# Kernel tuning notes

Measured on AMD Instinct MI355X. Metric: run time of the kernel, lower is better.

Reference implementation:

```python
import jax, jax.numpy as jnp
import numpy as np

EPS = 1e-5  # torch BatchNorm1d default eps

def _bn(x, g, b):
    # BatchNorm1d in training mode: batch mean, biased variance
    m = jnp.mean(x, axis=0)
    v = jnp.mean((x - m) ** 2, axis=0)
    return g * (x - m) * jax.lax.rsqrt(v + EPS) + b

N_ENT, N_REL = 50000, 200
D_E = D_R = 32
RANK = 32
NI = 1024  # must satisfy NI**2 == D_R * D_E**3
B = 64

def setup_inputs() -> dict:
    key = jax.random.key(0)
    ks = jax.random.split(key, 10)
    s = 0.001
    inp = {
        "E": s * jax.random.normal(ks[0], (N_ENT, D_E), jnp.float32),
        "R": s * jax.random.normal(ks[1], (N_REL, D_R), jnp.float32),
        "U_root": s * jax.random.normal(ks[2], (N_REL, RANK, RANK), jnp.float32),
        "U12": s * jax.random.normal(ks[3], (RANK, NI, NI), jnp.float32),
        "U3R": s * jax.random.normal(ks[4], (RANK, NI, NI), jnp.float32),
        "P": s * jax.random.normal(ks[5], (RANK, D_E), jnp.float32),
        "g_r": jnp.ones((D_R,), jnp.float32), "b_r": jnp.zeros((D_R,), jnp.float32),
        "g_e": jnp.ones((D_E,), jnp.float32), "b_e": jnp.zeros((D_E,), jnp.float32),
        "g_w": jnp.ones((D_E,), jnp.float32), "b_w": jnp.zeros((D_E,), jnp.float32),
        "r_idx": jax.random.randint(ks[6], (B,), 0, N_REL),
        "e2_idx": jax.random.randint(ks[7], (B,), 0, N_ENT),
        "e3_idx": jax.random.randint(ks[8], (B,), 0, N_ENT),
        "miss_ent_domain": 3,
    }
    return inp

def reference(E, R, U_root, U12, U3R, P, g_r, b_r, g_e, b_e, g_w, b_w,
              r_idx, e2_idx, e3_idx, miss_ent_domain):
    Bsz = r_idx.shape[0]
    d_r, d_e = R.shape[1], E.shape[1]

    r_emb = _bn(R[r_idx], g_r, b_r)                      # (B, d_r)

    # einsum 'brs,ria,rjb,rkc->bijk' with P.unsqueeze(1): the dangling
    # indices s, a, b, c are each summed out independently, so the
    # contraction factorizes into rank-1 pieces over r.
    a = U_root[r_idx].sum(-1)                            # (B, r)
    u12 = U12.sum(-1)                                    # (r, ni)
    u3 = U3R.sum(-1)                                     # (r, ni)
    p = P.sum(-1)                                        # (r,)
    W = jnp.einsum('br,ri,rj,r->bij', a, u12, u3, p)     # (B, ni, ni)
    W = W.reshape(Bsz, d_r, d_e, d_e, d_e)               # implicit HT core

    # bmm(r_emb (B,1,d_r), W (B,d_r,-1))
    W_mat = jnp.einsum('bd,bdijk->bijk', r_emb, W)       # (B, d_e, d_e, d_e)

    e2 = _bn(E[e2_idx], g_e, b_e)                        # (B, d_e)
    e3 = _bn(E[e3_idx], g_e, b_e)                        # (B, d_e)

    if miss_ent_domain == 1:
        vec = jnp.einsum('bijk,bk,bj->bi', W_mat, e3, e2)
    elif miss_ent_domain == 2:
        vec = jnp.einsum('bijk,bk,bi->bj', W_mat, e3, e2)
    else:
        vec = jnp.einsum('bijk,bi,bj->bk', W_mat, e2, e3)

    vec = _bn(vec, g_w, b_w)                             # (B, d_e)
    logits = vec @ E.T                                   # (B, |E|)
    return jax.nn.softmax(logits, axis=1)
```

## Files before the change

### kernel.cpp

```cpp
#include <hip/hip_runtime.h>
#include <math.h>

#define NENT 50000
#define DD   32
#define BSZ  64
#define NI   1024
#define NROWS 65536
#define EPS  1e-5f

#define WS_U12S 0
#define WS_U3S  32768
#define WS_P    65536
#define WS_A    65568
#define WS_RE   67616
#define WS_E2   69664
#define WS_E3   71712
#define WS_VEC  73760
#define WS_SUM  75808
#define WS_VECN 75872
#define WS_PART 77920
#define NCHUNK  196

__device__ void bn_block(const float* __restrict__ src, const int* __restrict__ idx,
                         const float* __restrict__ g, const float* __restrict__ bb,
                         float* __restrict__ dst, float* xs, float* st) {
    for (int i = threadIdx.x; i < BSZ * DD; i += 256) {
        int b = i >> 5, d = i & 31;
        xs[i] = src[(size_t)idx[b] * DD + d];
    }
    __syncthreads();
    if (threadIdx.x < DD) {
        int d = threadIdx.x;
        float m = 0.f;
        for (int b = 0; b < BSZ; ++b) m += xs[b * 32 + d];
        m *= (1.f / 64.f);
        float v = 0.f;
        for (int b = 0; b < BSZ; ++b) { float t = xs[b * 32 + d] - m; v += t * t; }
        v *= (1.f / 64.f);
        st[d]      = m;
        st[32 + d] = g[d] / sqrtf(v + EPS);
    }
    __syncthreads();
    for (int i = threadIdx.x; i < BSZ * DD; i += 256) {
        int d = i & 31;
        dst[i] = (xs[i] - st[d]) * st[32 + d] + bb[d];
    }
    __syncthreads();
}

#define HADD4(v) (((v).x + (v).y) + ((v).z + (v).w))

#define LOADP(p, buf) do {                                                      \
    const float4* _s = (((p) < 4)                                               \
        ? (u12v + (((size_t)(p) * 4096 + (size_t)w) * 512))                     \
        : (u3v  + (((size_t)((p) - 4) * 4096 + (size_t)w) * 512))) + lane;      \
    _Pragma("unroll")                                                           \
    for (int _i = 0; _i < 8; ++_i) (buf)[_i] = _s[(size_t)_i * 64];             \
} while (0)

#define REDSTORE(p, buf) do {                                                   \
    float _sa = HADD4((buf)[0]) + HADD4((buf)[1]) + HADD4((buf)[2]) + HADD4((buf)[3]); \
    float _sb = HADD4((buf)[4]) + HADD4((buf)[5]) + HADD4((buf)[6]) + HADD4((buf)[7]); \
    float _mine  = (lane < 32) ? _sa : _sb;                                     \
    float _other = __shfl_xor((lane < 32) ? _sb : _sa, 32, 64);                 \
    float _comb = _mine + _other;                                               \
    _Pragma("unroll")                                                           \
    for (int _o = 16; _o; _o >>= 1) _comb += __shfl_xor(_comb, _o, 64);         \
    int _grow = ((p) * 4096 + w) * 2;                                           \
    if (lane == 0)  ws[_grow]     = _comb;                                      \
    if (lane == 32) ws[_grow + 1] = _comb;                                      \
} while (0)

__global__ __launch_bounds__(256, 4) void k1_rowsums(
    const float* __restrict__ U12, const float* __restrict__ U3R,
    const float* __restrict__ R, const float* __restrict__ E,
    const float* __restrict__ U_root, const float* __restrict__ P,
    const float* __restrict__ g_r, const float* __restrict__ b_r,
    const float* __restrict__ g_e, const float* __restrict__ b_e,
    const int* __restrict__ r_idx, const int* __restrict__ e2_idx,
    const int* __restrict__ e3_idx, float* __restrict__ ws) {
    __shared__ float xs[BSZ * DD];
    __shared__ float st[64];
    int blk = blockIdx.x;
    if (blk < 1024) {
        int w = blk * 4 + (threadIdx.x >> 6);
        int lane = threadIdx.x & 63;
        const float4* u12v = (const float4*)U12;
        const float4* u3v  = (const float4*)U3R;
        float4 A[8], Bv[8];
        LOADP(0, A);
        LOADP(1, Bv);
#pragma unroll
        for (int p = 0; p < 8; p += 2) {
            if (p + 2 < 8) { REDSTORE(p, A); LOADP(p + 2, A); }
            else            REDSTORE(p, A);
            if (p + 3 < 8) { REDSTORE(p + 1, Bv); LOADP(p + 3, Bv); }
            else            REDSTORE(p + 1, Bv);
        }
        return;
    }
    int tid = threadIdx.x;
    float* wp   = ws + WS_P;
    float* wa   = ws + WS_A;
    float* wvec = ws + WS_VEC;
    if (tid < 32) {
        float s = 0.f;
#pragma unroll
        for (int c = 0; c < 32; ++c) s += P[tid * 32 + c];
        wp[tid] = s;
    }
    for (int i = tid; i < BSZ * DD; i += 256) {
        int b = i >> 5, r = i & 31;
        const float* u = U_root + (size_t)r_idx[b] * (DD * DD) + r * 32;
        float s = 0.f;
#pragma unroll
        for (int c = 0; c < 32; ++c) s += u[c];
        wa[i]   = s;
        wvec[i] = 0.f;
    }
    bn_block(R, r_idx,  g_r, b_r, ws + WS_RE, xs, st);
    bn_block(E, e2_idx, g_e, b_e, ws + WS_E2, xs, st);
    bn_block(E, e3_idx, g_e, b_e, ws + WS_E3, xs, st);
}

__global__ __launch_bounds__(256) void k2b_core(float* __restrict__ ws) {
    const float* u12s = ws + WS_U12S;
    const float* u3s  = ws + WS_U3S;
    const float* wp   = ws + WS_P;
    const float* wa   = ws + WS_A;
    const float* wre  = ws + WS_RE;
    const float* we2  = ws + WS_E2;
    const float* we3  = ws + WS_E3;
    float* wvec = ws + WS_VEC;
    int lane = threadIdx.x & 63;
    int pair = blockIdx.x * 4 + (threadIdx.x >> 6);
    int b = pair >> 5, r = pair & 31;
    float e2v = we2[b * 32 + (lane & 31)];
    const float* u12r = u12s + r * NI;
    float acc = 0.f;
#pragma unroll
    for (int t = 0; t < 16; ++t) {
        int di = t * 64 + lane;
        acc += u12r[di] * wre[b * 32 + (di >> 5)] * e2v;
    }
#pragma unroll
    for (int o = 32; o; o >>= 1) acc += __shfl_xor(acc, o, 64);
    int k = lane & 31, j0 = (lane >> 5) * 16;
    const float* u3r = u3s + r * NI;
    float bacc = 0.f;
#pragma unroll
    for (int jj = 0; jj < 16; ++jj) {
        int j = j0 + jj;
        bacc += we3[b * 32 + j] * u3r[j * 32 + k];
    }
    bacc += __shfl_down(bacc, 32, 64);
    if (lane < 32) {
        float coef = wa[b * 32 + r] * wp[r] * acc;
        atomicAdd(&wvec[b * 32 + k], coef * bacc);
    }
}

__global__ __launch_bounds__(256) void k3a_sums(const float* __restrict__ E,
                                                const float* __restrict__ g_w,
                                                const float* __restrict__ b_w,
                                                float* __restrict__ ws) {
    __shared__ float vs[BSZ * DD];
    __shared__ float st[64];
    __shared__ float part[4][32];
    const float* wvec = ws + WS_VEC;
    int t = threadIdx.x;
    for (int i = t; i < BSZ * DD; i += 256) vs[i] = wvec[i];
    __syncthreads();
    if (t < DD) {
        float m = 0.f;
        for (int b = 0; b < BSZ; ++b) m += vs[b * 32 + t];
        m *= (1.f / 64.f);
        float v = 0.f;
        for (int b = 0; b < BSZ; ++b) { float d = vs[b * 32 + t] - m; v += d * d; }
        v *= (1.f / 64.f);
        st[t]      = m;
        st[32 + t] = g_w[t] / sqrtf(v + EPS);
    }
    __syncthreads();
    for (int i = t; i < BSZ * DD; i += 256) {
        int d = i & 31;
        vs[i] = (vs[i] - st[d]) * st[32 + d] + b_w[d];
    }
    __syncthreads();
    int q = blockIdx.x;
    int nchunk = q >> 1, b0 = (q & 1) * 32;
    int n = nchunk * 256 + t;
    int lane = t & 63, w = t >> 6;
    bool valid = n < NENT;
    int nc = valid ? n : (NENT - 1);
    float4 er[8];
    const float4* ep = (const float4*)(E + (size_t)nc * DD);
#pragma unroll
    for (int qq = 0; qq < 8; ++qq) er[qq] = ep[qq];
    float pacc = 0.f;
#pragma unroll 4
    for (int j = 0; j < 32; ++j) {
        int b = b0 + j;
        const float4* vp = (const float4*)(vs + b * 32);
        float acc = 0.f;
#pragma unroll
        for (int qq = 0; qq < 8; ++qq) {
            float4 vv = vp[qq];
            acc += er[qq].x * vv.x + er[qq].y * vv.y + er[qq].z * vv.z + er[qq].w * vv.w;
        }
        float e = valid ? __expf(acc) : 0.f;
#pragma unroll
        for (int o = 32; o; o >>= 1) e += __shfl_xor(e, o, 64);
        pacc = (lane == j) ? e : pacc;
    }
    if (lane < 32) part[w][lane] = pacc;
    __syncthreads();
    if (t < 32) {
        float s = part[0][t] + part[1][t] + part[2][t] + part[3][t];
        ws[WS_PART + nchunk * 64 + b0 + t] = s;
    }
}

__global__ __launch_bounds__(256) void k3b_finish(const float* __restrict__ g_w,
                                                  const float* __restrict__ b_w,
                                                  float* __restrict__ ws) {
    __shared__ float red[4][64];
    __shared__ float xs[BSZ * DD];
    __shared__ float st[64];
    int t = threadIdx.x;
    int b = t & 63, chunk = t >> 6;
    const float* pp = ws + WS_PART;
    float s = 0.f;
    for (int p = chunk * 49; p < chunk * 49 + 49; ++p) s += pp[p * 64 + b];
    red[chunk][b] = s;
    const float* wvec = ws + WS_VEC;
    for (int i = t; i < BSZ * DD; i += 256) xs[i] = wvec[i];
    __syncthreads();
    if (t < 64) {
        float tot = red[0][t] + red[1][t] + red[2][t] + red[3][t];
        ws[WS_SUM + t] = 1.0f / tot;
    }
    if (t < DD) {
        float m = 0.f;
        for (int bb = 0; bb < BSZ; ++bb) m += xs[bb * 32 + t];
        m *= (1.f / 64.f);
        float v = 0.f;
        for (int bb = 0; bb < BSZ; ++bb) { float d = xs[bb * 32 + t] - m; v += d * d; }
        v *= (1.f / 64.f);
        st[t]      = m;
        st[32 + t] = g_w[t] / sqrtf(v + EPS);
    }
    __syncthreads();
    for (int i = t; i < BSZ * DD; i += 256) {
        int d = i & 31;
        ws[WS_VECN + i] = (xs[i] - st[d]) * st[32 + d] + b_w[d];
    }
}

__global__ __launch_bounds__(256) void k3c_write(const float* __restrict__ E,
                                                 const float* __restrict__ ws,
                                                 float* __restrict__ out) {
    __shared__ float vs[BSZ * DD];
    __shared__ float iv[64];
    int t = threadIdx.x;
    for (int i = t; i < BSZ * DD; i += 256) vs[i] = ws[WS_VECN + i];
    if (t < 64) iv[t] = ws[WS_SUM + t];
    __syncthreads();
    int q = blockIdx.x;
    int nchunk = q >> 1, b0 = (q & 1) * 32;
    int n = nchunk * 256 + t;
    if (n >= NENT) return;
    float4 er[8];
    const float4* ep = (const float4*)(E + (size_t)n * DD);
#pragma unroll
    for (int qq = 0; qq < 8; ++qq) er[qq] = ep[qq];
#pragma unroll 4
    for (int j = 0; j < 32; ++j) {
        int b = b0 + j;
        const float4* vp = (const float4*)(vs + b * 32);
        float acc = 0.f;
#pragma unroll
        for (int qq = 0; qq < 8; ++qq) {
            float4 vv = vp[qq];
            acc += er[qq].x * vv.x + er[qq].y * vv.y + er[qq].z * vv.z + er[qq].w * vv.w;
        }
        out[(size_t)b * NENT + n] = __expf(acc) * iv[b];
    }
}

extern "C" void kernel_launch(void* const* d_in, const int* in_sizes, int n_in,
                              void* d_out, int out_size, void* d_ws, size_t ws_size,
                              hipStream_t stream) {
    (void)in_sizes; (void)n_in; (void)out_size; (void)ws_size;
    const float* E      = (const float*)d_in[0];
    const float* R      = (const float*)d_in[1];
    const float* U_root = (const float*)d_in[2];
    const float* U12    = (const float*)d_in[3];
    const float* U3R    = (const float*)d_in[4];
    const float* P      = (const float*)d_in[5];
    const float* g_r    = (const float*)d_in[6];
    const float* b_r    = (const float*)d_in[7];
    const float* g_e    = (const float*)d_in[8];
    const float* b_e    = (const float*)d_in[9];
    const float* g_w    = (const float*)d_in[10];
    const float* b_w    = (const float*)d_in[11];
    const int* r_idx    = (const int*)d_in[12];
    const int* e2_idx   = (const int*)d_in[13];
    const int* e3_idx   = (const int*)d_in[14];
    float* ws  = (float*)d_ws;
    float* out = (float*)d_out;

    k1_rowsums<<<dim3(1025), dim3(256), 0, stream>>>(
        U12, U3R, R, E, U_root, P, g_r, b_r, g_e, b_e, r_idx, e2_idx, e3_idx, ws);
    k2b_core<<<dim3(512), dim3(256), 0, stream>>>(ws);
    k3a_sums<<<dim3(2 * NCHUNK), dim3(256), 0, stream>>>(E, g_w, b_w, ws);
    k3b_finish<<<dim3(1), dim3(256), 0, stream>>>(g_w, b_w, ws);
    k3c_write<<<dim3(2 * NCHUNK), dim3(256), 0, stream>>>(E, ws, out);
}
```

Before: 362.7 us.

## Fuse core, softmax sums and output write into one persistent kernel with grid barriers

Merges the four post-rowsum kernels into a single 512-block kernel that uses two software grid barriers. The logits are kept in registers between the softmax sum pass and the output write, so E is not reloaded or recomputed. The big U12/U3R streaming loads also become nontemporal. This removes three launches and the duplicated logit computation, but relies on all 512 blocks being co-resident and on a spin barrier with a timeout guard, which could silently break correctness.

```diff
diff --git a/kernel.cpp b/kernel.cpp
--- a/kernel.cpp
+++ b/kernel.cpp
@@ -16,10 +16,28 @@
 #define WS_E2   69664
 #define WS_E3   71712
 #define WS_VEC  73760
-#define WS_SUM  75808
-#define WS_VECN 75872
+#define WS_BAR0 75808
+#define WS_BAR1 75824
 #define WS_PART 77920
 #define NCHUNK  196
+#define NBLK2   512
+
+typedef float v4 __attribute__((ext_vector_type(4)));
+
+__device__ __forceinline__ void grid_barrier(unsigned* cnt, unsigned nblk) {
+    __syncthreads();
+    if (threadIdx.x == 0) {
+        __threadfence();
+        __hip_atomic_fetch_add(cnt, 1u, __ATOMIC_RELEASE, __HIP_MEMORY_SCOPE_AGENT);
+        long guard = 0;
+        while (__hip_atomic_load(cnt, __ATOMIC_RELAXED, __HIP_MEMORY_SCOPE_AGENT) < nblk
+               && ++guard < (1L << 20)) {
+            __builtin_amdgcn_s_sleep(8);
+        }
+    }
+    __syncthreads();
+    __threadfence();
+}
 
 __device__ void bn_block(const float* __restrict__ src, const int* __restrict__ idx,
                          const float* __restrict__ g, const float* __restrict__ bb,
@@ -48,14 +66,15 @@
     __syncthreads();
 }
 
-#define HADD4(v) (((v).x + (v).y) + ((v).z + (v).w))
+#define HADD4(v) ((((v)[0]) + ((v)[1])) + (((v)[2]) + ((v)[3])))
 
 #define LOADP(p, buf) do {                                                      \
-    const float4* _s = (((p) < 4)                                               \
+    const v4* _s = (((p) < 4)                                                   \
         ? (u12v + (((size_t)(p) * 4096 + (size_t)w) * 512))                     \
         : (u3v  + (((size_t)((p) - 4) * 4096 + (size_t)w) * 512))) + lane;      \
     _Pragma("unroll")                                                           \
-    for (int _i = 0; _i < 8; ++_i) (buf)[_i] = _s[(size_t)_i * 64];             \
+    for (int _i = 0; _i < 8; ++_i)                                              \
+        (buf)[_i] = __builtin_nontemporal_load(_s + (size_t)_i * 64);           \
 } while (0)
 
 #define REDSTORE(p, buf) do {                                                   \
@@ -85,9 +104,9 @@
     if (blk < 1024) {
         int w = blk * 4 + (threadIdx.x >> 6);
         int lane = threadIdx.x & 63;
-        const float4* u12v = (const float4*)U12;
-        const float4* u3v  = (const float4*)U3R;
-        float4 A[8], Bv[8];
+        const v4* u12v = (const v4*)U12;
+        const v4* u3v  = (const v4*)U3R;
+        v4 A[8], Bv[8];
         LOADP(0, A);
         LOADP(1, Bv);
 #pragma unroll
@@ -103,6 +122,10 @@
     float* wp   = ws + WS_P;
     float* wa   = ws + WS_A;
     float* wvec = ws + WS_VEC;
+    if (tid == 0) {
+        ((unsigned*)ws)[WS_BAR0] = 0u;
+        ((unsigned*)ws)[WS_BAR1] = 0u;
+    }
     if (tid < 32) {
         float s = 0.f;
 #pragma unroll
@@ -123,168 +146,128 @@
     bn_block(E, e3_idx, g_e, b_e, ws + WS_E3, xs, st);
 }
 
-__global__ __launch_bounds__(256) void k2b_core(float* __restrict__ ws) {
-    const float* u12s = ws + WS_U12S;
-    const float* u3s  = ws + WS_U3S;
-    const float* wp   = ws + WS_P;
-    const float* wa   = ws + WS_A;
-    const float* wre  = ws + WS_RE;
-    const float* we2  = ws + WS_E2;
-    const float* we3  = ws + WS_E3;
-    float* wvec = ws + WS_VEC;
-    int lane = threadIdx.x & 63;
-    int pair = blockIdx.x * 4 + (threadIdx.x >> 6);
-    int b = pair >> 5, r = pair & 31;
-    float e2v = we2[b * 32 + (lane & 31)];
-    const float* u12r = u12s + r * NI;
-    float acc = 0.f;
-#pragma unroll
-    for (int t = 0; t < 16; ++t) {
-        int di = t * 64 + lane;
-        acc += u12r[di] * wre[b * 32 + (di >> 5)] * e2v;
-    }
-#pragma unroll
-    for (int o = 32; o; o >>= 1) acc += __shfl_xor(acc, o, 64);
-    int k = lane & 31, j0 = (lane >> 5) * 16;
-    const float* u3r = u3s + r * NI;
-    float bacc = 0.f;
-#pragma unroll
-    for (int jj = 0; jj < 16; ++jj) {
-        int j = j0 + jj;
-        bacc += we3[b * 32 + j] * u3r[j * 32 + k];
-    }
-    bacc += __shfl_down(bacc, 32, 64);
-    if (lane < 32) {
-        float coef = wa[b * 32 + r] * wp[r] * acc;
-        atomicAdd(&wvec[b * 32 + k], coef * bacc);
-    }
-}
-
-__global__ __launch_bounds__(256) void k3a_sums(const float* __restrict__ E,
-                                                const float* __restrict__ g_w,
-                                                const float* __restrict__ b_w,
-                                                float* __restrict__ ws) {
+__global__ __launch_bounds__(256, 2) void k2_fused(
+    const float* __restrict__ E, const float* __restrict__ g_w,
+    const float* __restrict__ b_w, float* __restrict__ ws,
+    float* __restrict__ out) {
+    const int t = threadIdx.x;
+    const int lane = t & 63;
+    const int wid  = t >> 6;
+
+    {
+        const float* u12s = ws + WS_U12S;
+        const float* u3s  = ws + WS_U3S;
+        const float* wp   = ws + WS_P;
+        const float* wa   = ws + WS_A;
+        const float* wre  = ws + WS_RE;
+        const float* we2  = ws + WS_E2;
+        const float* we3  = ws + WS_E3;
+        float* wvec = ws + WS_VEC;
+        int pair = blockIdx.x * 4 + wid;
+        int b = pair >> 5, r = pair & 31;
+        float e2v = we2[b * 32 + (lane & 31)];
+        const float* u12r = u12s + r * NI;
+        float acc = 0.f;
+#pragma unroll
+        for (int tt = 0; tt < 16; ++tt) {
+            int di = tt * 64 + lane;
+            acc += u12r[di] * wre[b * 32 + (di >> 5)] * e2v;
+        }
+#pragma unroll
+        for (int o = 32; o; o >>= 1) acc += __shfl_xor(acc, o, 64);
+        int k = lane & 31, j0 = (lane >> 5) * 16;
+        const float* u3r = u3s + r * NI;
+        float bacc = 0.f;
+#pragma unroll
+        for (int jj = 0; jj < 16; ++jj) {
+            int j = j0 + jj;
+            bacc += we3[b * 32 + j] * u3r[j * 32 + k];
+        }
+        bacc += __shfl_down(bacc, 32, 64);
+        if (lane < 32) {
+            float coef = wa[b * 32 + r] * wp[r] * acc;
+            atomicAdd(&wvec[b * 32 + k], coef * bacc);
+        }
+    }
+    grid_barrier((unsigned*)ws + WS_BAR0, NBLK2);
+
     __shared__ float vs[BSZ * DD];
     __shared__ float st[64];
     __shared__ float part[4][32];
-    const float* wvec = ws + WS_VEC;
-    int t = threadIdx.x;
-    for (int i = t; i < BSZ * DD; i += 256) vs[i] = wvec[i];
-    __syncthreads();
-    if (t < DD) {
-        float m = 0.f;
-        for (int b = 0; b < BSZ; ++b) m += vs[b * 32 + t];
-        m *= (1.f / 64.f);
-        float v = 0.f;
-        for (int b = 0; b < BSZ; ++b) { float d = vs[b * 32 + t] - m; v += d * d; }
-        v *= (1.f / 64.f);
-        st[t]      = m;
-        st[32 + t] = g_w[t] / sqrtf(v + EPS);
-    }
-    __syncthreads();
-    for (int i = t; i < BSZ * DD; i += 256) {
-        int d = i & 31;
-        vs[i] = (vs[i] - st[d]) * st[32 + d] + b_w[d];
-    }
-    __syncthreads();
-    int q = blockIdx.x;
-    int nchunk = q >> 1, b0 = (q & 1) * 32;
-    int n = nchunk * 256 + t;
-    int lane = t & 63, w = t >> 6;
-    bool valid = n < NENT;
-    int nc = valid ? n : (NENT - 1);
-    float4 er[8];
-    const float4* ep = (const float4*)(E + (size_t)nc * DD);
-#pragma unroll
-    for (int qq = 0; qq < 8; ++qq) er[qq] = ep[qq];
-    float pacc = 0.f;
-#pragma unroll 4
-    for (int j = 0; j < 32; ++j) {
-        int b = b0 + j;
-        const float4* vp = (const float4*)(vs + b * 32);
-        float acc = 0.f;
-#pragma unroll
-        for (int qq = 0; qq < 8; ++qq) {
-            float4 vv = vp[qq];
-            acc += er[qq].x * vv.x + er[qq].y * vv.y + er[qq].z * vv.z + er[qq].w * vv.w;
-        }
-        float e = valid ? __expf(acc) : 0.f;
-#pragma unroll
-        for (int o = 32; o; o >>= 1) e += __shfl_xor(e, o, 64);
-        pacc = (lane == j) ? e : pacc;
-    }
-    if (lane < 32) part[w][lane] = pacc;
-    __syncthreads();
-    if (t < 32) {
-        float s = part[0][t] + part[1][t] + part[2][t] + part[3][t];
-        ws[WS_PART + nchunk * 64 + b0 + t] = s;
-    }
-}
-
-__global__ __launch_bounds__(256) void k3b_finish(const float* __restrict__ g_w,
-                                                  const float* __restrict__ b_w,
-                                                  float* __restrict__ ws) {
-    __shared__ float red[4][64];
-    __shared__ float xs[BSZ * DD];
-    __shared__ float st[64];
-    int t = threadIdx.x;
-    int b = t & 63, chunk = t >> 6;
-    const float* pp = ws + WS_PART;
-    float s = 0.f;
-    for (int p = chunk * 49; p < chunk * 49 + 49; ++p) s += pp[p * 64 + b];
-    red[chunk][b] = s;
-    const float* wvec = ws + WS_VEC;
-    for (int i = t; i < BSZ * DD; i += 256) xs[i] = wvec[i];
-    __syncthreads();
+    {
+        const float* wvec = ws + WS_VEC;
+        for (int i = t; i < BSZ * DD; i += 256) vs[i] = wvec[i];
+        __syncthreads();
+        if (t < DD) {
+            float m = 0.f;
+            for (int b = 0; b < BSZ; ++b) m += vs[b * 32 + t];
+            m *= (1.f / 64.f);
+            float v = 0.f;
+            for (int b = 0; b < BSZ; ++b) { float d = vs[b * 32 + t] - m; v += d * d; }
+            v *= (1.f / 64.f);
+            st[t]      = m;
+            st[32 + t] = g_w[t] / sqrtf(v + EPS);
+        }
+        __syncthreads();
+        for (int i = t; i < BSZ * DD; i += 256) {
+            int d = i & 31;
+            vs[i] = (vs[i] - st[d]) * st[32 + d] + b_w[d];
+        }
+        __syncthreads();
+    }
+    const int q = blockIdx.x;
+    const bool active = q < 2 * NCHUNK;
+    const int nchunk = q >> 1, b0 = (q & 1) * 32;
+    const int n = nchunk * 256 + t;
+    const bool valid = active && (n < NENT);
+    float accs[32];
+    if (active) {
+        int nc = valid ? n : (NENT - 1);
+        float4 er[8];
+        const float4* ep = (const float4*)(E + (size_t)nc * DD);
+#pragma unroll
+        for (int qq = 0; qq < 8; ++qq) er[qq] = ep[qq];
+        float pacc = 0.f;
+#pragma unroll
+        for (int j = 0; j < 32; ++j) {
+            const float4* vp = (const float4*)(vs + (b0 + j) * 32);
+            float acc = 0.f;
+#pragma unroll
+            for (int qq = 0; qq < 8; ++qq) {
+                float4 vv = vp[qq];
+                acc += er[qq].x * vv.x + er[qq].y * vv.y + er[qq].z * vv.z + er[qq].w * vv.w;
+            }
+            accs[j] = acc;
+            float e = valid ? __expf(acc) : 0.f;
+#pragma unroll
+            for (int o = 32; o; o >>= 1) e += __shfl_xor(e, o, 64);
+            pacc = (lane == j) ? e : pacc;
+        }
+        if (lane < 32) part[wid][lane] = pacc;
+        __syncthreads();
+        if (t < 32) {
+            float s = part[0][t] + part[1][t] + part[2][t] + part[3][t];
+            ws[WS_PART + (size_t)(b0 + t) * NCHUNK + nchunk] = s;
+        }
+    }
+    grid_barrier((unsigned*)ws + WS_BAR1, NBLK2);
+
+    __shared__ float iv[64];
     if (t < 64) {
-        float tot = red[0][t] + red[1][t] + red[2][t] + red[3][t];
-        ws[WS_SUM + t] = 1.0f / tot;
-    }
-    if (t < DD) {
-        float m = 0.f;
-        for (int bb = 0; bb < BSZ; ++bb) m += xs[bb * 32 + t];
-        m *= (1.f / 64.f);
-        float v = 0.f;
-        for (int bb = 0; bb < BSZ; ++bb) { float d = xs[bb * 32 + t] - m; v += d * d; }
-        v *= (1.f / 64.f);
-        st[t]      = m;
-        st[32 + t] = g_w[t] / sqrtf(v + EPS);
-    }
-    __syncthreads();
-    for (int i = t; i < BSZ * DD; i += 256) {
-        int d = i & 31;
-        ws[WS_VECN + i] = (xs[i] - st[d]) * st[32 + d] + b_w[d];
-    }
-}
-
-__global__ __launch_bounds__(256) void k3c_write(const float* __restrict__ E,
-                                                 const float* __restrict__ ws,
-                                                 float* __restrict__ out) {
-    __shared__ float vs[BSZ * DD];
-    __shared__ float iv[64];
-    int t = threadIdx.x;
-    for (int i = t; i < BSZ * DD; i += 256) vs[i] = ws[WS_VECN + i];
-    if (t < 64) iv[t] = ws[WS_SUM + t];
-    __syncthreads();
-    int q = blockIdx.x;
-    int nchunk = q >> 1, b0 = (q & 1) * 32;
-    int n = nchunk * 256 + t;
-    if (n >= NENT) return;
-    float4 er[8];
-    const float4* ep = (const float4*)(E + (size_t)n * DD);
-#pragma unroll
-    for (int qq = 0; qq < 8; ++qq) er[qq] = ep[qq];
-#pragma unroll 4
-    for (int j = 0; j < 32; ++j) {
-        int b = b0 + j;
-        const float4* vp = (const float4*)(vs + b * 32);
-        float acc = 0.f;
-#pragma unroll
-        for (int qq = 0; qq < 8; ++qq) {
-            float4 vv = vp[qq];
-            acc += er[qq].x * vv.x + er[qq].y * vv.y + er[qq].z * vv.z + er[qq].w * vv.w;
-        }
-        out[(size_t)b * NENT + n] = __expf(acc) * iv[b];
+        const float4* pb = (const float4*)(ws + WS_PART + (size_t)t * NCHUNK);
+        float s = 0.f;
+#pragma unroll 7
+        for (int p = 0; p < 49; ++p) {
+            float4 v = pb[p];
+            s += (v.x + v.y) + (v.z + v.w);
+        }
+        iv[t] = 1.0f / s;
+    }
+    __syncthreads();
+    if (valid) {
+#pragma unroll
+        for (int j = 0; j < 32; ++j)
+            out[(size_t)(b0 + j) * NENT + n] = __expf(accs[j]) * iv[b0 + j];
     }
 }
 
@@ -312,8 +295,5 @@
 
     k1_rowsums<<<dim3(1025), dim3(256), 0, stream>>>(
         U12, U3R, R, E, U_root, P, g_r, b_r, g_e, b_e, r_idx, e2_idx, e3_idx, ws);
-    k2b_core<<<dim3(512), dim3(256), 0, stream>>>(ws);
-    k3a_sums<<<dim3(2 * NCHUNK), dim3(256), 0, stream>>>(E, g_w, b_w, ws);
-    k3b_finish<<<dim3(1), dim3(256), 0, stream>>>(g_w, b_w, ws);
-    k3c_write<<<dim3(2 * NCHUNK), dim3(256), 0, stream>>>(E, ws, out);
-}
+    k2_fused<<<dim3(NBLK2), dim3(256), 0, stream>>>(E, g_w, b_w, ws, out);
+}
```

Measured after the change: 444.5 us. 22.5% more time.
